# Kernel optimization log

Hardware: AMD Instinct MI355X
Metric: run time of the kernel (lower is better)

## Reference

```python
import jax, jax.numpy as jnp
import numpy as np

NUM_TYPES = 1000  # num_edge_type (static for segment_sum)


def setup_inputs() -> dict:
    key = jax.random.key(0)
    k1, k2, k3, k4, k5 = jax.random.split(key, 5)
    N = 1_000_000          # batch of edges
    D = 256                # embed_size
    ATTR_NUM = 200_000     # base_node_num - c_num - e_num
    TOTAL_ATTRS = 50_000   # sum of ragged attr-list lengths over types (~50/type)
    data = jax.random.randint(k1, (N,), 0, NUM_TYPES, dtype=jnp.int64) if jax.config.jax_enable_x64 else jax.random.randint(k1, (N,), 0, NUM_TYPES, dtype=jnp.int32)
    attr_table = jax.random.normal(k2, (ATTR_NUM, D), dtype=jnp.float32)
    edge_type_embedding = jax.random.normal(k3, (NUM_TYPES, D), dtype=jnp.float32)
    flat_attr_ids = jax.random.randint(k4, (TOTAL_ATTRS,), 0, ATTR_NUM, dtype=jnp.int32)
    attr_seg_ids = jax.random.randint(k5, (TOTAL_ATTRS,), 0, NUM_TYPES, dtype=jnp.int32)
    return {
        "data": data,
        "attr_table": attr_table,
        "edge_type_embedding": edge_type_embedding,
        "flat_attr_ids": flat_attr_ids,
        "attr_seg_ids": attr_seg_ids,
    }


def reference(data, attr_table, edge_type_embedding, flat_attr_ids, attr_seg_ids):
    # Per-type bag-sum of attribute embeddings (ragged gather + segment reduce).
    # type_attr_sum[t] == sum_{a in type2attr[t]} attr_emb[a]; empty types -> 0,
    # which matches the original's self.zero_attr fallback.
    gathered = attr_table[flat_attr_ids]                          # [T_attrs, D]
    type_attr_sum = jax.ops.segment_sum(gathered, attr_seg_ids,
                                        num_segments=NUM_TYPES)   # [NUM_TYPES, D]
    # fusion_type == 'add': edge-type embedding + summed attr embeddings per edge
    return edge_type_embedding[data] + type_attr_sum[data]        # [N, D]
```

## Files before the change

kernel.cpp:

```cpp
#include <hip/hip_runtime.h>


#define EE_D   256
#define EE_D4  64
#define EE_NT  1000
#define EE_K   4

typedef float fvec4 __attribute__((ext_vector_type(4)));

__global__ __launch_bounds__(256) void ee_build_comb(
        const fvec4* __restrict__ ete,
        const fvec4* __restrict__ attr,
        const int* __restrict__ ids,
        const int* __restrict__ segs,
        fvec4* __restrict__ comb, int na) {
    const int t0   = blockIdx.x * EE_K;
    const int tid  = threadIdx.x;
    const int wave = tid >> 6;
    const int lane = tid & 63;

    fvec4 acc[EE_K];
    #pragma unroll
    for (int k = 0; k < EE_K; ++k) acc[k] = (fvec4)0.f;

    for (int base = wave * 64; base < na; base += 256) {
        int a = base + lane;
        int s = -1, id = 0;
        if (a < na) { s = segs[a]; id = ids[a]; }
        #pragma unroll
        for (int k = 0; k < EE_K; ++k) {
            unsigned long long m = __ballot(s == t0 + k);
            while (m) {
                int j = __ffsll((long long)m) - 1;
                m &= m - 1;
                int aid = __shfl(id, j);
                acc[k] += attr[(size_t)aid * EE_D4 + lane];
            }
        }
    }

    __shared__ fvec4 red[EE_K][4][64];
    #pragma unroll
    for (int k = 0; k < EE_K; ++k) red[k][wave][lane] = acc[k];
    __syncthreads();
    if (wave < EE_K) {
        int k = wave;
        fvec4 r = red[k][0][lane];
        #pragma unroll
        for (int w = 1; w < 4; ++w) r += red[k][w][lane];
        r += ete[(size_t)(t0 + k) * EE_D4 + lane];
        comb[(size_t)(t0 + k) * EE_D4 + lane] = r;
    }
}

__global__ __launch_bounds__(256) void ee_gather_out(
        const int* __restrict__ data,
        const fvec4* __restrict__ comb,
        fvec4* __restrict__ out, int n) {
    const int gid  = blockIdx.x * blockDim.x + threadIdx.x;
    const int wave = gid >> 6;
    const int lane = gid & 63;
    const int nw   = (gridDim.x * blockDim.x) >> 6;

    for (int base = wave * 64; base < n; base += nw * 64) {
        int r = base + lane;
        int idx = (r < n) ? __builtin_nontemporal_load(&data[r]) : 0;
        int lim = n - base;
        if (lim >= 64) {
            #pragma unroll
            for (int j = 0; j < 64; ++j) {
                int t = __builtin_amdgcn_readlane(idx, j);
                fvec4 v = comb[(size_t)t * EE_D4 + lane];
                __builtin_nontemporal_store(v, &out[(size_t)(base + j) * EE_D4 + lane]);
            }
        } else {
            for (int j = 0; j < lim; ++j) {
                int t = __shfl(idx, j);
                fvec4 v = comb[(size_t)t * EE_D4 + lane];
                __builtin_nontemporal_store(v, &out[(size_t)(base + j) * EE_D4 + lane]);
            }
        }
    }
}

extern "C" void kernel_launch(void* const* d_in, const int* in_sizes, int n_in,
                              void* d_out, int out_size, void* d_ws, size_t ws_size,
                              hipStream_t stream) {
    const int*   data          = (const int*)d_in[0];
    const float* attr_table    = (const float*)d_in[1];
    const float* ete           = (const float*)d_in[2];
    const int*   flat_attr_ids = (const int*)d_in[3];
    const int*   attr_seg_ids  = (const int*)d_in[4];
    fvec4* comb = (fvec4*)d_ws;
    int N  = in_sizes[0];
    int TA = in_sizes[3];

    ee_build_comb<<<EE_NT / EE_K, 256, 0, stream>>>(
        (const fvec4*)ete, (const fvec4*)attr_table,
        flat_attr_ids, attr_seg_ids, comb, TA);

    ee_gather_out<<<2048, 256, 0, stream>>>(
        data, comb, (fvec4*)d_out, N);
}
```

Baseline: 256.6 us.

## Bucket output rows by edge type and scatter combined rows per type

Replaces the per-row gather of combined type embeddings with a counting-sort pipeline: a histogram of edge types, a prefix scan, a scatter of row ids into per-type lists, then one block per type writing its register-held combined row to every output row of that type. The aim is to avoid repeated reads of the combined table by keeping each type's row in registers. In exchange it adds four extra kernel launches, global atomics and an extra pass over the index array. Output writes become random-row scatters rather than sequential streams. The old gather path remains as a fallback when workspace is too small.

Measured after the change: 496.2 us. 1.93x slower.

```diff
diff --git a/kernel.cpp b/kernel.cpp
--- a/kernel.cpp
+++ b/kernel.cpp
@@ -1,7 +1,6 @@
 #include <hip/hip_runtime.h>
 
 
-#define EE_D   256
 #define EE_D4  64
 #define EE_NT  1000
 #define EE_K   4
@@ -53,6 +52,80 @@
     }
 }
 
+__global__ void ee_zero(int* __restrict__ p, int n) {
+    int i = blockIdx.x * blockDim.x + threadIdx.x;
+    if (i < n) p[i] = 0;
+}
+
+__global__ __launch_bounds__(256) void ee_hist(const int* __restrict__ data, int n,
+                                               int* __restrict__ hist) {
+    __shared__ int lh[EE_NT];
+    for (int i = threadIdx.x; i < EE_NT; i += 256) lh[i] = 0;
+    __syncthreads();
+    for (int r = blockIdx.x * blockDim.x + threadIdx.x; r < n; r += gridDim.x * blockDim.x)
+        atomicAdd(&lh[data[r]], 1);
+    __syncthreads();
+    for (int i = threadIdx.x; i < EE_NT; i += 256) {
+        int c = lh[i];
+        if (c) atomicAdd(&hist[i], c);
+    }
+}
+
+__global__ __launch_bounds__(1024) void ee_scan(const int* __restrict__ hist,
+                                                int* __restrict__ start) {
+    __shared__ int a[1024], b[1024];
+    int tid = threadIdx.x;
+    a[tid] = (tid < EE_NT) ? hist[tid] : 0;
+    __syncthreads();
+    int* src = a; int* dst = b;
+    #pragma unroll
+    for (int off = 1; off < 1024; off <<= 1) {
+        int v = src[tid];
+        if (tid >= off) v += src[tid - off];
+        dst[tid] = v;
+        __syncthreads();
+        int* t = src; src = dst; dst = t;
+    }
+    if (tid <= EE_NT) start[tid] = (tid == 0) ? 0 : src[tid - 1];
+}
+
+__global__ __launch_bounds__(256) void ee_scatter_ids(const int* __restrict__ data, int n,
+        const int* __restrict__ start, int* __restrict__ cursor, int* __restrict__ rowlist) {
+    for (int r = blockIdx.x * blockDim.x + threadIdx.x; r < n; r += gridDim.x * blockDim.x) {
+        int t = data[r];
+        int pos = atomicAdd(&cursor[t], 1);
+        rowlist[start[t] + pos] = r;
+    }
+}
+
+__global__ __launch_bounds__(256) void ee_scatter_out(const fvec4* __restrict__ comb,
+        const int* __restrict__ start, const int* __restrict__ rowlist,
+        fvec4* __restrict__ out) {
+    const int t    = blockIdx.x;
+    const int wave = threadIdx.x >> 6;
+    const int lane = threadIdx.x & 63;
+    const int s = start[t], e = start[t + 1];
+    const fvec4 v = comb[(size_t)t * EE_D4 + lane];
+
+    for (int base = s + wave * 64; base < e; base += 256) {
+        int i = base + lane;
+        int rid = (i < e) ? rowlist[i] : 0;
+        int lim = e - base;
+        if (lim >= 64) {
+            #pragma unroll
+            for (int j = 0; j < 64; ++j) {
+                int r = __builtin_amdgcn_readlane(rid, j);
+                __builtin_nontemporal_store(v, &out[(size_t)r * EE_D4 + lane]);
+            }
+        } else {
+            for (int j = 0; j < lim; ++j) {
+                int r = __shfl(rid, j);
+                __builtin_nontemporal_store(v, &out[(size_t)r * EE_D4 + lane]);
+            }
+        }
+    }
+}
+
 __global__ __launch_bounds__(256) void ee_gather_out(
         const int* __restrict__ data,
         const fvec4* __restrict__ comb,
@@ -91,14 +164,28 @@
     const float* ete           = (const float*)d_in[2];
     const int*   flat_attr_ids = (const int*)d_in[3];
     const int*   attr_seg_ids  = (const int*)d_in[4];
-    fvec4* comb = (fvec4*)d_ws;
     int N  = in_sizes[0];
     int TA = in_sizes[3];
+
+    char* ws = (char*)d_ws;
+    fvec4* comb    = (fvec4*)ws;
+    int*   hist    = (int*)(ws + (1 << 20));
+    int*   cursor  = hist + 1024;
+    int*   start   = cursor + 1024;
+    int*   rowlist = start + 1024;
+    size_t need = (1 << 20) + 3 * 4096 + (size_t)N * 4;
 
     ee_build_comb<<<EE_NT / EE_K, 256, 0, stream>>>(
         (const fvec4*)ete, (const fvec4*)attr_table,
         flat_attr_ids, attr_seg_ids, comb, TA);
 
-    ee_gather_out<<<2048, 256, 0, stream>>>(
-        data, comb, (fvec4*)d_out, N);
+    if (ws_size >= need) {
+        ee_zero<<<8, 256, 0, stream>>>(hist, 2048);
+        ee_hist<<<128, 256, 0, stream>>>(data, N, hist);
+        ee_scan<<<1, 1024, 0, stream>>>(hist, start);
+        ee_scatter_ids<<<1024, 256, 0, stream>>>(data, N, start, cursor, rowlist);
+        ee_scatter_out<<<EE_NT, 256, 0, stream>>>(comb, start, rowlist, (fvec4*)d_out);
+    } else {
+        ee_gather_out<<<2048, 256, 0, stream>>>(data, comb, (fvec4*)d_out, N);
+    }
 }
```
